# Optimization experiments

Hardware: AMD Instinct MI355X
Metric: run time of the kernel (lower is better)

The kernel has to match this reference:

```python
import jax, jax.numpy as jnp
import numpy as np

SEQ_LEN = 4096
D_MODEL = 1024
NUM_POLES = 64


def setup_inputs() -> dict:
    key = jax.random.key(0)
    k1, k2, k3 = jax.random.split(key, 3)
    z = jax.random.normal(k1, (SEQ_LEN,), dtype=jnp.float32)
    poles = jax.random.normal(k2, (D_MODEL, NUM_POLES), dtype=jnp.float32) * 0.1
    residues = jax.random.normal(k3, (D_MODEL, NUM_POLES), dtype=jnp.float32) * 0.01
    return {"z": z, "poles": poles, "residues": residues}


def reference(z, poles, residues):
    # z: (S,), poles/residues: (D, P) -> out: (S, D)
    # Cauchy sum: out[s, d] = sum_p residues[d, p] / (z[s] - poles[d, p])
    denom = z[:, None, None] - poles[None, :, :]          # (S, D, P)
    result = jnp.sum(residues[None, :, :] / denom, axis=-1)  # (S, D)
    return result
```

## Files before the change

kernel.cpp:

```cpp
#include <hip/hip_runtime.h>
#include <hip/hip_bf16.h>

#define S_TOTAL 4096
#define D_TOTAL 1024
#define NPOLES  64
#define NPAIRS  32
#define D_PER_BLOCK 64
#define S_PER_BLOCK 64
#define BLOCK 256
#define ZG 8

__device__ __forceinline__ float sanitize_finite(float x) {
    const float lim = 1.0e38f;
    const unsigned u = __float_as_uint(x);
    if ((u & 0x7f800000u) == 0x7f800000u)
        return (u & 0x80000000u) ? -lim : lim;
    return fminf(fmaxf(x, -lim), lim);
}

__global__ __launch_bounds__(BLOCK, 4) void cauchy_lds_kernel(
    const float* __restrict__ z,
    const float* __restrict__ poles,
    const float* __restrict__ residues,
    float* __restrict__ out)
{
    const int tid  = threadIdx.x;
    const int lane = tid & 63;
    const int w    = tid >> 6;
    const int dl   = lane & 15;
    const int q    = lane >> 4;
    const int d0   = blockIdx.y * D_PER_BLOCK;
    const int s0   = blockIdx.x * S_PER_BLOCK;

    __shared__ float4 cpair[NPAIRS][D_PER_BLOCK];

    {
        const int dF = tid & 63;
        const int hq = tid >> 6;
        const float* pp = poles    + (size_t)(d0 + dF) * NPOLES + hq * 16;
        const float* rr = residues + (size_t)(d0 + dF) * NPOLES + hq * 16;
#pragma unroll
        for (int k = 0; k < 4; ++k) {
            const float4 p4 = *reinterpret_cast<const float4*>(pp + 4 * k);
            const float4 r4 = *reinterpret_cast<const float4*>(rr + 4 * k);
            const int pq = hq * 8 + 2 * k;
            cpair[pq + 0][dF] = make_float4(r4.x + r4.y,
                                            -fmaf(r4.x, p4.y, r4.y * p4.x),
                                            p4.x + p4.y, p4.x * p4.y);
            cpair[pq + 1][dF] = make_float4(r4.z + r4.w,
                                            -fmaf(r4.z, p4.w, r4.w * p4.z),
                                            p4.z + p4.w, p4.z * p4.w);
        }
    }
    __syncthreads();

    const int myd  = d0 + w * 16 + dl;
    const int widx = w * 16 + dl;

    for (int g = 0; g < S_PER_BLOCK / ZG; ++g) {
        const int sb = s0 + g * ZG;
        const float z0 = z[sb + 0], z1 = z[sb + 1], z2 = z[sb + 2], z3 = z[sb + 3];
        const float z4 = z[sb + 4], z5 = z[sb + 5], z6 = z[sb + 6], z7 = z[sb + 7];
        float a0 = 0.f, a1 = 0.f, a2 = 0.f, a3 = 0.f;
        float a4 = 0.f, a5 = 0.f, a6 = 0.f, a7 = 0.f;
#pragma unroll
        for (int k = 0; k < NPAIRS / 4; ++k) {
            const float4 c = cpair[q * 8 + k][widx];
            const float A = c.x, B = c.y, S = c.z, P = c.w;
#define TERM(zz, aa)                                                        \
            {   const float den = fmaf(zz, zz - S, P);                      \
                aa = fmaf(fmaf(A, zz, B), __builtin_amdgcn_rcpf(den), aa); }
            TERM(z0, a0) TERM(z1, a1) TERM(z2, a2) TERM(z3, a3)
            TERM(z4, a4) TERM(z5, a5) TERM(z6, a6) TERM(z7, a7)
#undef TERM
        }
#define RED(aa) aa += __shfl_xor(aa, 16, 64); aa += __shfl_xor(aa, 32, 64);
        RED(a0) RED(a1) RED(a2) RED(a3) RED(a4) RED(a5) RED(a6) RED(a7)
#undef RED
        const float v0 = (q == 0) ? a0 : (q == 1) ? a1 : (q == 2) ? a2 : a3;
        const float v1 = (q == 0) ? a4 : (q == 1) ? a5 : (q == 2) ? a6 : a7;
        out[(size_t)(sb + q) * D_TOTAL + myd]     = sanitize_finite(v0);
        out[(size_t)(sb + 4 + q) * D_TOTAL + myd] = sanitize_finite(v1);
    }
}

extern "C" void kernel_launch(void* const* d_in, const int* in_sizes, int n_in,
                              void* d_out, int out_size, void* d_ws, size_t ws_size,
                              hipStream_t stream) {
    const float* z        = (const float*)d_in[0];
    const float* poles    = (const float*)d_in[1];
    const float* residues = (const float*)d_in[2];
    float* out            = (float*)d_out;

    dim3 grid(S_TOTAL / S_PER_BLOCK, D_TOTAL / D_PER_BLOCK);
    dim3 block(BLOCK);
    cauchy_lds_kernel<<<grid, block, 0, stream>>>(z, poles, residues, out);
}
```

Before: 88.29 us.

## Merge pole pairs into degree-16 rational function evaluated with packed Horner

Each thread combines its 16 poles and residues into one numerator and denominator polynomial through a tree of polynomial products. It then evaluates both per z value with packed fp32 FMAs and a single reciprocal, replacing eight per-pair reciprocals read from LDS. The LDS staging and barrier are removed, and the s-tile is halved to add more blocks. The high-degree polynomial form risks numerical error near poles, and the per-thread merge setup adds cost that is amortized over fewer z values.

Measured after the change: 80.15 us. 1.1x faster.

```diff
diff --git a/kernel.cpp b/kernel.cpp
--- a/kernel.cpp
+++ b/kernel.cpp
@@ -4,11 +4,14 @@
 #define S_TOTAL 4096
 #define D_TOTAL 1024
 #define NPOLES  64
-#define NPAIRS  32
 #define D_PER_BLOCK 64
-#define S_PER_BLOCK 64
+#define S_PER_BLOCK 32
 #define BLOCK 256
 #define ZG 8
+
+typedef float f32x2 __attribute__((ext_vector_type(2)));
+
+__device__ __forceinline__ f32x2 splat2(float s) { f32x2 v; v.x = s; v.y = s; return v; }
 
 __device__ __forceinline__ float sanitize_finite(float x) {
     const float lim = 1.0e38f;
@@ -18,7 +21,28 @@
     return fminf(fmaxf(x, -lim), lim);
 }
 
-__global__ __launch_bounds__(BLOCK, 4) void cauchy_lds_kernel(
+template <int N>
+__device__ __forceinline__ void mergeN(const float* nA, const float* dA,
+                                       const float* nB, const float* dB,
+                                       float* nO, float* dO) {
+#pragma unroll
+    for (int k = 0; k < 2 * N; ++k) { dO[k] = 0.f; nO[k] = 0.f; }
+#pragma unroll
+    for (int i = 0; i < N; ++i)
+#pragma unroll
+        for (int j = 0; j < N; ++j) {
+            dO[i + j] = fmaf(dA[i], dB[j], dO[i + j]);
+            nO[i + j] = fmaf(nA[i], dB[j], nO[i + j]);
+            nO[i + j] = fmaf(nB[i], dA[j], nO[i + j]);
+        }
+#pragma unroll
+    for (int k = 0; k < N; ++k) {
+        dO[N + k] += dA[k] + dB[k];
+        nO[N + k] += nA[k] + nB[k];
+    }
+}
+
+__global__ __launch_bounds__(BLOCK, 4) void cauchy_deg16_kernel(
     const float* __restrict__ z,
     const float* __restrict__ poles,
     const float* __restrict__ residues,
@@ -31,54 +55,79 @@
     const int q    = lane >> 4;
     const int d0   = blockIdx.y * D_PER_BLOCK;
     const int s0   = blockIdx.x * S_PER_BLOCK;
+    const int widx = w * 16 + dl;
+    const int myd  = d0 + widx;
 
-    __shared__ float4 cpair[NPAIRS][D_PER_BLOCK];
-
+    float p[16], r[16];
     {
-        const int dF = tid & 63;
-        const int hq = tid >> 6;
-        const float* pp = poles    + (size_t)(d0 + dF) * NPOLES + hq * 16;
-        const float* rr = residues + (size_t)(d0 + dF) * NPOLES + hq * 16;
+        const float* pp = poles    + (size_t)myd * NPOLES + q * 16;
+        const float* rr = residues + (size_t)myd * NPOLES + q * 16;
 #pragma unroll
         for (int k = 0; k < 4; ++k) {
             const float4 p4 = *reinterpret_cast<const float4*>(pp + 4 * k);
             const float4 r4 = *reinterpret_cast<const float4*>(rr + 4 * k);
-            const int pq = hq * 8 + 2 * k;
-            cpair[pq + 0][dF] = make_float4(r4.x + r4.y,
-                                            -fmaf(r4.x, p4.y, r4.y * p4.x),
-                                            p4.x + p4.y, p4.x * p4.y);
-            cpair[pq + 1][dF] = make_float4(r4.z + r4.w,
-                                            -fmaf(r4.z, p4.w, r4.w * p4.z),
-                                            p4.z + p4.w, p4.z * p4.w);
+            p[4 * k + 0] = p4.x; p[4 * k + 1] = p4.y;
+            p[4 * k + 2] = p4.z; p[4 * k + 3] = p4.w;
+            r[4 * k + 0] = r4.x; r[4 * k + 1] = r4.y;
+            r[4 * k + 2] = r4.z; r[4 * k + 3] = r4.w;
         }
     }
-    __syncthreads();
-
-    const int myd  = d0 + w * 16 + dl;
-    const int widx = w * 16 + dl;
+    float n1[8][2], d1[8][2];
+#pragma unroll
+    for (int j = 0; j < 8; ++j) {
+        const float pa = p[2 * j], pb = p[2 * j + 1];
+        const float ra = r[2 * j], rb = r[2 * j + 1];
+        n1[j][1] = ra + rb;
+        n1[j][0] = -fmaf(ra, pb, rb * pa);
+        d1[j][1] = -(pa + pb);
+        d1[j][0] = pa * pb;
+    }
+    float n2[4][4], d2[4][4];
+#pragma unroll
+    for (int j = 0; j < 4; ++j)
+        mergeN<2>(n1[2 * j], d1[2 * j], n1[2 * j + 1], d1[2 * j + 1], n2[j], d2[j]);
+    float n3[2][8], d3[2][8];
+#pragma unroll
+    for (int j = 0; j < 2; ++j)
+        mergeN<4>(n2[2 * j], d2[2 * j], n2[2 * j + 1], d2[2 * j + 1], n3[j], d3[j]);
+    float n4[16], d4[16];
+    mergeN<8>(n3[0], d3[0], n3[1], d3[1], n4, d4);
 
     for (int g = 0; g < S_PER_BLOCK / ZG; ++g) {
         const int sb = s0 + g * ZG;
-        const float z0 = z[sb + 0], z1 = z[sb + 1], z2 = z[sb + 2], z3 = z[sb + 3];
-        const float z4 = z[sb + 4], z5 = z[sb + 5], z6 = z[sb + 6], z7 = z[sb + 7];
-        float a0 = 0.f, a1 = 0.f, a2 = 0.f, a3 = 0.f;
-        float a4 = 0.f, a5 = 0.f, a6 = 0.f, a7 = 0.f;
+        f32x2 zz[4], acc[4];
 #pragma unroll
-        for (int k = 0; k < NPAIRS / 4; ++k) {
-            const float4 c = cpair[q * 8 + k][widx];
-            const float A = c.x, B = c.y, S = c.z, P = c.w;
-#define TERM(zz, aa)                                                        \
-            {   const float den = fmaf(zz, zz - S, P);                      \
-                aa = fmaf(fmaf(A, zz, B), __builtin_amdgcn_rcpf(den), aa); }
-            TERM(z0, a0) TERM(z1, a1) TERM(z2, a2) TERM(z3, a3)
-            TERM(z4, a4) TERM(z5, a5) TERM(z6, a6) TERM(z7, a7)
-#undef TERM
+        for (int t = 0; t < 4; ++t) {
+            zz[t].x = z[sb + 2 * t];
+            zz[t].y = z[sb + 2 * t + 1];
+            acc[t] = splat2(0.f);
         }
-#define RED(aa) aa += __shfl_xor(aa, 16, 64); aa += __shfl_xor(aa, 32, 64);
-        RED(a0) RED(a1) RED(a2) RED(a3) RED(a4) RED(a5) RED(a6) RED(a7)
-#undef RED
-        const float v0 = (q == 0) ? a0 : (q == 1) ? a1 : (q == 2) ? a2 : a3;
-        const float v1 = (q == 0) ? a4 : (q == 1) ? a5 : (q == 2) ? a6 : a7;
+#pragma unroll
+        for (int t = 0; t < 4; ++t) {
+            f32x2 h = zz[t] + splat2(d4[15]);
+#pragma unroll
+            for (int i = 14; i >= 0; --i)
+                h = __builtin_elementwise_fma(h, zz[t], splat2(d4[i]));
+            f32x2 n = __builtin_elementwise_fma(splat2(n4[15]), zz[t], splat2(n4[14]));
+#pragma unroll
+            for (int i = 13; i >= 0; --i)
+                n = __builtin_elementwise_fma(n, zz[t], splat2(n4[i]));
+            f32x2 rc;
+            rc.x = __builtin_amdgcn_rcpf(h.x);
+            rc.y = __builtin_amdgcn_rcpf(h.y);
+            acc[t] = __builtin_elementwise_fma(n, rc, acc[t]);
+        }
+#pragma unroll
+        for (int t = 0; t < 4; ++t) {
+            acc[t].x += __shfl_xor(acc[t].x, 16, 64);
+            acc[t].y += __shfl_xor(acc[t].y, 16, 64);
+            acc[t].x += __shfl_xor(acc[t].x, 32, 64);
+            acc[t].y += __shfl_xor(acc[t].y, 32, 64);
+        }
+        const float v0 = (q == 0) ? acc[0].x : (q == 1) ? acc[0].y
+                       : (q == 2) ? acc[1].x : acc[1].y;
+        const float v1 = (q == 0) ? acc[2].x : (q == 1) ? acc[2].y
+                       : (q == 2) ? acc[3].x : acc[3].y;
         out[(size_t)(sb + q) * D_TOTAL + myd]     = sanitize_finite(v0);
         out[(size_t)(sb + 4 + q) * D_TOTAL + myd] = sanitize_finite(v1);
     }
@@ -94,5 +143,5 @@
 
     dim3 grid(S_TOTAL / S_PER_BLOCK, D_TOTAL / D_PER_BLOCK);
     dim3 block(BLOCK);
-    cauchy_lds_kernel<<<grid, block, 0, stream>>>(z, poles, residues, out);
+    cauchy_deg16_kernel<<<grid, block, 0, stream>>>(z, poles, residues, out);
 }
```
